# Kernel optimization log

Measured on AMD Instinct MI355X. Metric: run time of the kernel, lower is better.

The kernel has to match this reference:

```python
import jax, jax.numpy as jnp
import numpy as np

B, H, W = 64, 512, 512
T = 100           # num_thresholds
R = 8             # defect regions per image (max label id)
BLOCK = 128       # defect regions are 128x128 blocks on a 4x4 grid
SAT = 1.0         # saturation_threshold (relative)


def setup_inputs() -> dict:
    key = jax.random.key(0)
    k1, _ = jax.random.split(key)
    preds = jax.random.uniform(k1, (B, H, W), dtype=jnp.float32)
    thresholds = jnp.linspace(0.0, 1.0, T).astype(jnp.float32)
    # Build a labeled GT mask: R disjoint 128x128 block regions per image,
    # labels 1..R (0 = background). This plays the role of measure.label(target).
    rng = np.random.default_rng(0)
    labels = np.zeros((B, H, W), dtype=np.int32)
    gb = H // BLOCK           # 4 blocks per side -> 16 candidate blocks
    nblocks = gb * gb
    for b in range(B):
        chosen = rng.permutation(nblocks)[:R]
        for rid, blk in enumerate(chosen, start=1):
            r, c = divmod(int(blk), gb)
            labels[b, r * BLOCK:(r + 1) * BLOCK, c * BLOCK:(c + 1) * BLOCK] = rid
    return {"preds": preds, "thresholds": thresholds, "labels": jnp.asarray(labels)}


def reference(preds, thresholds, labels):
    # preds: (B,H,W) float32 in [0,1); thresholds: (T,) sorted; labels: (B,H,W) int32, 0=bg.
    Bn, Hn, Wn = preds.shape
    Tn = thresholds.shape[0]
    flat_s = preds.reshape(-1)
    flat_l = labels.reshape(-1)
    # bucket[p] = number of thresholds <= score[p]; pixel passes thr[t] iff bucket > t.
    bucket = jnp.searchsorted(thresholds, flat_s, side='right')  # int in [0, T]
    # ---- background FP / TN per threshold (exact counts via histogram) ----
    bg = (flat_l == 0).astype(jnp.int32)
    bg_hist = jax.ops.segment_sum(bg, bucket, num_segments=Tn + 1)  # (T+1,)
    bg_total = bg_hist.sum()
    fp = (bg_total - jnp.cumsum(bg_hist)[:Tn]).astype(jnp.float32)  # fp[t] = #bg with score>=thr[t]
    tn = bg_total.astype(jnp.float32) - fp
    # ---- per-region TP per threshold (segmented histogram) ----
    bidx = jnp.repeat(jnp.arange(Bn), Hn * Wn)
    seg = bidx * R + (flat_l - 1)              # region id in [0, B*R)
    comb = seg * (Tn + 1) + bucket
    NSEG = Bn * R * (Tn + 1)
    comb = jnp.where(flat_l > 0, comb, NSEG)   # dump bg pixels in overflow slot
    hist = jax.ops.segment_sum(jnp.ones_like(bucket, dtype=jnp.int32), comb,
                               num_segments=NSEG + 1)[:NSEG].reshape(Bn, R, Tn + 1)
    area = hist.sum(-1)                                       # (B,R) defect areas
    tp = (area[..., None] - jnp.cumsum(hist, -1)[..., :Tn]).astype(jnp.float32)  # (B,R,T)
    sat = jnp.maximum(area.astype(jnp.float32) * SAT, 1.0)    # relative saturation
    valid = (area > 0).astype(jnp.float32)                    # guard empty regions
    spro = jnp.minimum(tp / sat[..., None], 1.0) * valid[..., None]
    spro_sum = spro.sum((0, 1))                               # (T,)
    n_def = jnp.maximum(valid.sum(), 1.0)
    mean_spro = spro_sum / n_def
    # ---- AUC over FPR (max_fpr = 1.0) ----
    denom = fp + tn
    fpr = jnp.where(denom > 0, fp / jnp.maximum(denom, 1.0), 0.0)
    order = jnp.argsort(fpr)
    x = fpr[order]
    y = mean_spro[order]
    auc = jnp.sum((x[1:] - x[:-1]) * (y[1:] + y[:-1]) * 0.5)  # trapezoid rule
    return auc
```

## Files before the change

### kernel.cpp

```cpp
#include <hip/hip_runtime.h>

#define B_N 64
#define H_N 512
#define W_N 512
#define T_N 100
#define TB  101
#define R_N 8
#define NLAB 9
#define BLOCKS_PER_IMG 32
#define PIX_PER_IMG (H_N * W_N)
#define PIX_PER_BLOCK (PIX_PER_IMG / BLOCKS_PER_IMG)

__device__ __forceinline__ int bucket_of(float s) {
    const double C = 1.0 / 99.0;
    int k0 = (int)(s * 99.0f) + 1;
    float tlo = (float)((double)(k0 - 1) * C);
    float thi = (float)((double)k0 * C);
    return k0 - (s < tlo ? 1 : 0) + (s >= thi ? 1 : 0);
}

__global__ __launch_bounds__(256) void hist_kernel(
    const float* __restrict__ preds, const int* __restrict__ labels,
    int* __restrict__ region_hist,
    int* __restrict__ bg_hist)
{
    __shared__ int whist[4][NLAB * TB];

    const int tid  = threadIdx.x;
    const int wave = tid >> 6;

    for (int i = tid; i < 4 * NLAB * TB; i += 256) ((int*)whist)[i] = 0;
    __syncthreads();

    const int img   = blockIdx.x / BLOCKS_PER_IMG;
    const int chunk = blockIdx.x % BLOCKS_PER_IMG;
    const long base = (long)img * PIX_PER_IMG + (long)chunk * PIX_PER_BLOCK;
    const float4* p4 = (const float4*)(preds + base);
    const int4*   l4 = (const int4*)(labels + base);
    int* __restrict__ myh = whist[wave];

    const int iters = PIX_PER_BLOCK / (256 * 8);

    float4 pa = p4[tid], pb = p4[256 + tid];
    int4   la = l4[tid], lb = l4[256 + tid];
    for (int it = 0; it < iters; ++it) {
        float4 na, nb; int4 nla, nlb;
        if (it + 1 < iters) {
            int o = (it * 2 + 2) * 256 + tid;
            na  = p4[o]; nb  = p4[o + 256];
            nla = l4[o]; nlb = l4[o + 256];
        }
        float ps[8] = {pa.x, pa.y, pa.z, pa.w, pb.x, pb.y, pb.z, pb.w};
        int   ls[8] = {la.x, la.y, la.z, la.w, lb.x, lb.y, lb.z, lb.w};
#pragma unroll
        for (int j = 0; j < 8; ++j)
            atomicAdd(&myh[ls[j] * TB + bucket_of(ps[j])], 1);
        pa = na; pb = nb; la = nla; lb = nlb;
    }
    __syncthreads();

    for (int i = tid; i < NLAB * TB; i += 256) {
        int v = whist[0][i] + whist[1][i] + whist[2][i] + whist[3][i];
        if (v) {
            int lab = i / TB;
            int t   = i - lab * TB;
            if (lab == 0)
                atomicAdd(&bg_hist[img * TB + t], v);
            else
                atomicAdd(&region_hist[(img * R_N + (lab - 1)) * TB + t], v);
        }
    }
}

__global__ __launch_bounds__(256) void post_kernel(
    const int* __restrict__ region_hist,
    const int* __restrict__ bg_hist,
    float* __restrict__ spro_sum,
    int* __restrict__ n_def,
    int* __restrict__ done_ctr,
    float* __restrict__ out)
{
    __shared__ int   h_sh[R_N * TB];
    __shared__ float area_sh[R_N];
    __shared__ int   last_sh;
    const int img = blockIdx.x;
    const int tid = threadIdx.x;

    for (int i = tid; i < R_N * TB; i += 256)
        h_sh[i] = region_hist[img * (R_N * TB) + i];
    __syncthreads();

    if (tid < R_N) {
        int a = 0;
        for (int t = 0; t < TB; ++t) a += h_sh[tid * TB + t];
        area_sh[tid] = (float)a;
    }
    __syncthreads();

    if (tid < T_N) {
        float s = 0.0f;
#pragma unroll
        for (int r = 0; r < R_N; ++r) {
            int tp = 0;
            for (int k = tid + 1; k < TB; ++k) tp += h_sh[r * TB + k];
            float area  = area_sh[r];
            float sat   = fmaxf(area, 1.0f);
            float valid = (area > 0.0f) ? 1.0f : 0.0f;
            s += fminf((float)tp / sat, 1.0f) * valid;
        }
        atomicAdd(&spro_sum[tid], s);
    }
    if (tid == 0) {
        int v = 0;
        for (int r = 0; r < R_N; ++r) v += (area_sh[r] > 0.0f) ? 1 : 0;
        atomicAdd(n_def, v);
    }

    __syncthreads();
    if (tid == 0) {
        int prev = __hip_atomic_fetch_add(done_ctr, 1, __ATOMIC_ACQ_REL,
                                          __HIP_MEMORY_SCOPE_AGENT);
        last_sh = (prev == B_N - 1) ? 1 : 0;
    }
    __syncthreads();
    if (!last_sh) return;

    __shared__ int    stage[B_N * TB];
    __shared__ int    bgh[TB];
    __shared__ float  fpr_sh[T_N];
    __shared__ float  ms_sh[T_N];
    __shared__ int    order[T_N];
    __shared__ double contrib[T_N];

    for (int i = tid; i < B_N * TB; i += 256) stage[i] = bg_hist[i];
    __syncthreads();

    if (tid < TB) {
        int s = 0;
        for (int b = 0; b < B_N; ++b) s += stage[b * TB + tid];
        bgh[tid] = s;
    }
    __syncthreads();

    if (tid < T_N) {
        int fp_i = 0;
        for (int k = tid + 1; k < TB; ++k) fp_i += bgh[k];
        int tot = fp_i;
        for (int k = 0; k <= tid; ++k) tot += bgh[k];
        float bgt = (float)tot;
        float fp  = (float)fp_i;
        fpr_sh[tid] = (bgt > 0.0f) ? fp / fmaxf(bgt, 1.0f) : 0.0f;
        int   ndi = __hip_atomic_load(n_def, __ATOMIC_RELAXED, __HIP_MEMORY_SCOPE_AGENT);
        float ss  = __hip_atomic_load(&spro_sum[tid], __ATOMIC_RELAXED, __HIP_MEMORY_SCOPE_AGENT);
        float nd  = fmaxf((float)ndi, 1.0f);
        ms_sh[tid] = ss / nd;
    }
    __syncthreads();

    if (tid < T_N) {
        float v = fpr_sh[tid];
        int r = 0;
        for (int j = 0; j < T_N; ++j) {
            float u = fpr_sh[j];
            r += (u < v) | ((u == v) & (j < tid));
        }
        order[r] = tid;
    }
    __syncthreads();

    if (tid < T_N - 1) {
        int o0 = order[tid], o1 = order[tid + 1];
        double x0 = fpr_sh[o0], x1 = fpr_sh[o1];
        double y0 = ms_sh[o0],  y1 = ms_sh[o1];
        contrib[tid] = (x1 - x0) * (y0 + y1) * 0.5;
    } else if (tid < T_N) {
        contrib[tid] = 0.0;
    }
    __syncthreads();

    if (tid == 0) {
        double s = 0.0;
        for (int i = 0; i < T_N - 1; ++i) s += contrib[i];
        out[0] = (float)s;
    }
}

extern "C" void kernel_launch(void* const* d_in, const int* in_sizes, int n_in,
                              void* d_out, int out_size, void* d_ws, size_t ws_size,
                              hipStream_t stream) {
    const float* preds  = (const float*)d_in[0];
    const int*   labels = (const int*)d_in[2];
    float* out = (float*)d_out;

    int*   region_hist = (int*)d_ws;
    int*   bg_hist     = region_hist + B_N * R_N * TB;
    float* spro_sum    = (float*)(bg_hist + B_N * TB);
    int*   n_def       = (int*)(spro_sum + T_N);
    int*   done_ctr    = n_def + 1;

    size_t zbytes = sizeof(int) * (size_t)(B_N * R_N * TB + B_N * TB)
                  + sizeof(float) * T_N + 2 * sizeof(int);
    hipMemsetAsync(d_ws, 0, zbytes, stream);

    hist_kernel<<<B_N * BLOCKS_PER_IMG, 256, 0, stream>>>(preds, labels,
                                                          region_hist, bg_hist);
    post_kernel<<<B_N, 256, 0, stream>>>(region_hist, bg_hist, spro_sum,
                                         n_def, done_ctr, out);
}
```

Measured before the change: 168.1 us.

## Fuse histogram and post-processing into one cooperative kernel with grid syncs

Replaces the memset plus two kernel launches with a single cooperative kernel of 512 blocks. Each block zeroes part of the workspace, builds its shared-memory histogram, and the blocks then flush, reduce per image and compute the AUC between grid-wide syncs. This removes the launch and memset overhead and the last-block atomic counter. In exchange, each block now handles four times as many pixels, the software prefetch in the histogram loop is dropped, and three grid barriers are added. If the cooperative launch fails, a two-kernel path runs instead.

```diff
diff --git a/kernel.cpp b/kernel.cpp
--- a/kernel.cpp
+++ b/kernel.cpp
@@ -1,4 +1,7 @@
 #include <hip/hip_runtime.h>
+#include <hip/hip_cooperative_groups.h>
+
+namespace cg = cooperative_groups;
 
 #define B_N 64
 #define H_N 512
@@ -7,9 +10,15 @@
 #define TB  101
 #define R_N 8
 #define NLAB 9
-#define BLOCKS_PER_IMG 32
+#define NCOL (NLAB * TB)
 #define PIX_PER_IMG (H_N * W_N)
-#define PIX_PER_BLOCK (PIX_PER_IMG / BLOCKS_PER_IMG)
+
+#define CBLK_PER_IMG 8
+#define CGRID (B_N * CBLK_PER_IMG)
+#define CPIX (PIX_PER_IMG / CBLK_PER_IMG)
+#define FBLK_PER_IMG 32
+#define FGRID (B_N * FBLK_PER_IMG)
+#define FPIX (PIX_PER_IMG / FBLK_PER_IMG)
 
 __device__ __forceinline__ int bucket_of(float s) {
     const double C = 1.0 / 99.0;
@@ -19,144 +28,30 @@
     return k0 - (s < tlo ? 1 : 0) + (s >= thi ? 1 : 0);
 }
 
-__global__ __launch_bounds__(256) void hist_kernel(
-    const float* __restrict__ preds, const int* __restrict__ labels,
-    int* __restrict__ region_hist,
-    int* __restrict__ bg_hist)
-{
-    __shared__ int whist[4][NLAB * TB];
-
-    const int tid  = threadIdx.x;
-    const int wave = tid >> 6;
-
-    for (int i = tid; i < 4 * NLAB * TB; i += 256) ((int*)whist)[i] = 0;
-    __syncthreads();
-
-    const int img   = blockIdx.x / BLOCKS_PER_IMG;
-    const int chunk = blockIdx.x % BLOCKS_PER_IMG;
-    const long base = (long)img * PIX_PER_IMG + (long)chunk * PIX_PER_BLOCK;
+__device__ __forceinline__ void hist_phase(const float* __restrict__ preds,
+                                           const int* __restrict__ labels,
+                                           int* smem, int tid, int wave,
+                                           long base, int pix) {
     const float4* p4 = (const float4*)(preds + base);
     const int4*   l4 = (const int4*)(labels + base);
-    int* __restrict__ myh = whist[wave];
-
-    const int iters = PIX_PER_BLOCK / (256 * 8);
-
-    float4 pa = p4[tid], pb = p4[256 + tid];
-    int4   la = l4[tid], lb = l4[256 + tid];
+    int* myh = smem + wave * NCOL;
+    const int iters = pix / (256 * 8);
     for (int it = 0; it < iters; ++it) {
-        float4 na, nb; int4 nla, nlb;
-        if (it + 1 < iters) {
-            int o = (it * 2 + 2) * 256 + tid;
-            na  = p4[o]; nb  = p4[o + 256];
-            nla = l4[o]; nlb = l4[o + 256];
-        }
+        float4 pa = p4[(it * 2 + 0) * 256 + tid];
+        float4 pb = p4[(it * 2 + 1) * 256 + tid];
+        int4   la = l4[(it * 2 + 0) * 256 + tid];
+        int4   lb = l4[(it * 2 + 1) * 256 + tid];
         float ps[8] = {pa.x, pa.y, pa.z, pa.w, pb.x, pb.y, pb.z, pb.w};
         int   ls[8] = {la.x, la.y, la.z, la.w, lb.x, lb.y, lb.z, lb.w};
 #pragma unroll
         for (int j = 0; j < 8; ++j)
             atomicAdd(&myh[ls[j] * TB + bucket_of(ps[j])], 1);
-        pa = na; pb = nb; la = nla; lb = nlb;
-    }
-    __syncthreads();
-
-    for (int i = tid; i < NLAB * TB; i += 256) {
-        int v = whist[0][i] + whist[1][i] + whist[2][i] + whist[3][i];
-        if (v) {
-            int lab = i / TB;
-            int t   = i - lab * TB;
-            if (lab == 0)
-                atomicAdd(&bg_hist[img * TB + t], v);
-            else
-                atomicAdd(&region_hist[(img * R_N + (lab - 1)) * TB + t], v);
-        }
-    }
-}
-
-__global__ __launch_bounds__(256) void post_kernel(
-    const int* __restrict__ region_hist,
-    const int* __restrict__ bg_hist,
-    float* __restrict__ spro_sum,
-    int* __restrict__ n_def,
-    int* __restrict__ done_ctr,
-    float* __restrict__ out)
-{
-    __shared__ int   h_sh[R_N * TB];
-    __shared__ float area_sh[R_N];
-    __shared__ int   last_sh;
-    const int img = blockIdx.x;
-    const int tid = threadIdx.x;
-
-    for (int i = tid; i < R_N * TB; i += 256)
-        h_sh[i] = region_hist[img * (R_N * TB) + i];
-    __syncthreads();
-
-    if (tid < R_N) {
-        int a = 0;
-        for (int t = 0; t < TB; ++t) a += h_sh[tid * TB + t];
-        area_sh[tid] = (float)a;
-    }
-    __syncthreads();
-
-    if (tid < T_N) {
-        float s = 0.0f;
-#pragma unroll
-        for (int r = 0; r < R_N; ++r) {
-            int tp = 0;
-            for (int k = tid + 1; k < TB; ++k) tp += h_sh[r * TB + k];
-            float area  = area_sh[r];
-            float sat   = fmaxf(area, 1.0f);
-            float valid = (area > 0.0f) ? 1.0f : 0.0f;
-            s += fminf((float)tp / sat, 1.0f) * valid;
-        }
-        atomicAdd(&spro_sum[tid], s);
-    }
-    if (tid == 0) {
-        int v = 0;
-        for (int r = 0; r < R_N; ++r) v += (area_sh[r] > 0.0f) ? 1 : 0;
-        atomicAdd(n_def, v);
-    }
-
-    __syncthreads();
-    if (tid == 0) {
-        int prev = __hip_atomic_fetch_add(done_ctr, 1, __ATOMIC_ACQ_REL,
-                                          __HIP_MEMORY_SCOPE_AGENT);
-        last_sh = (prev == B_N - 1) ? 1 : 0;
-    }
-    __syncthreads();
-    if (!last_sh) return;
-
-    __shared__ int    stage[B_N * TB];
-    __shared__ int    bgh[TB];
-    __shared__ float  fpr_sh[T_N];
-    __shared__ float  ms_sh[T_N];
-    __shared__ int    order[T_N];
-    __shared__ double contrib[T_N];
-
-    for (int i = tid; i < B_N * TB; i += 256) stage[i] = bg_hist[i];
-    __syncthreads();
-
-    if (tid < TB) {
-        int s = 0;
-        for (int b = 0; b < B_N; ++b) s += stage[b * TB + tid];
-        bgh[tid] = s;
-    }
-    __syncthreads();
-
-    if (tid < T_N) {
-        int fp_i = 0;
-        for (int k = tid + 1; k < TB; ++k) fp_i += bgh[k];
-        int tot = fp_i;
-        for (int k = 0; k <= tid; ++k) tot += bgh[k];
-        float bgt = (float)tot;
-        float fp  = (float)fp_i;
-        fpr_sh[tid] = (bgt > 0.0f) ? fp / fmaxf(bgt, 1.0f) : 0.0f;
-        int   ndi = __hip_atomic_load(n_def, __ATOMIC_RELAXED, __HIP_MEMORY_SCOPE_AGENT);
-        float ss  = __hip_atomic_load(&spro_sum[tid], __ATOMIC_RELAXED, __HIP_MEMORY_SCOPE_AGENT);
-        float nd  = fmaxf((float)ndi, 1.0f);
-        ms_sh[tid] = ss / nd;
-    }
-    __syncthreads();
-
+    }
+}
+
+__device__ __forceinline__ void rank_sort_auc(int tid, const float* fpr_sh,
+                                              const float* ms_sh, int* order,
+                                              double* contrib, float* out) {
     if (tid < T_N) {
         float v = fpr_sh[tid];
         int r = 0;
@@ -167,7 +62,6 @@
         order[r] = tid;
     }
     __syncthreads();
-
     if (tid < T_N - 1) {
         int o0 = order[tid], o1 = order[tid + 1];
         double x0 = fpr_sh[o0], x1 = fpr_sh[o1];
@@ -177,12 +71,208 @@
         contrib[tid] = 0.0;
     }
     __syncthreads();
-
     if (tid == 0) {
         double s = 0.0;
         for (int i = 0; i < T_N - 1; ++i) s += contrib[i];
         out[0] = (float)s;
     }
+}
+
+__global__ __launch_bounds__(256) void fused_kernel(
+    const float* __restrict__ preds, const int* __restrict__ labels,
+    int*   __restrict__ rhist,
+    float* __restrict__ spro_part,
+    int*   __restrict__ validc,
+    float* __restrict__ out)
+{
+    cg::grid_group gg = cg::this_grid();
+    __shared__ __align__(16) int smem[4 * NCOL];
+
+    const int tid  = threadIdx.x;
+    const int bid  = blockIdx.x;
+    const int wave = tid >> 6;
+    const int gtid = bid * 256 + tid;
+
+    if (gtid < B_N * NCOL) rhist[gtid] = 0;
+
+    for (int i = tid; i < 4 * NCOL; i += 256) smem[i] = 0;
+    __syncthreads();
+
+    const int img   = bid / CBLK_PER_IMG;
+    const int chunk = bid % CBLK_PER_IMG;
+    hist_phase(preds, labels, smem, tid, wave,
+               (long)img * PIX_PER_IMG + (long)chunk * CPIX, CPIX);
+    __syncthreads();
+
+    gg.sync();
+
+    for (int i = tid; i < NCOL; i += 256) {
+        int v = smem[i] + smem[NCOL + i] + smem[2 * NCOL + i] + smem[3 * NCOL + i];
+        if (v) atomicAdd(&rhist[img * NCOL + i], v);
+    }
+
+    gg.sync();
+
+    if (bid < B_N) {
+        int*   h_sh    = smem;
+        float* area_sh = (float*)(smem + 912);
+        for (int i = tid; i < NCOL; i += 256) h_sh[i] = rhist[bid * NCOL + i];
+        __syncthreads();
+        if (tid < R_N) {
+            int a = 0;
+            for (int t = 0; t < TB; ++t) a += h_sh[(tid + 1) * TB + t];
+            area_sh[tid] = (float)a;
+        }
+        __syncthreads();
+        if (tid < T_N) {
+            float s = 0.0f;
+#pragma unroll
+            for (int r = 0; r < R_N; ++r) {
+                int tp = 0;
+                for (int k = tid + 1; k < TB; ++k) tp += h_sh[(r + 1) * TB + k];
+                float area  = area_sh[r];
+                float sat   = fmaxf(area, 1.0f);
+                float valid = (area > 0.0f) ? 1.0f : 0.0f;
+                s += fminf((float)tp / sat, 1.0f) * valid;
+            }
+            spro_part[bid * T_N + tid] = s;
+        }
+        if (tid == 0) {
+            int v = 0;
+            for (int r = 0; r < R_N; ++r) v += (area_sh[r] > 0.0f) ? 1 : 0;
+            validc[bid] = v;
+        }
+    }
+
+    gg.sync();
+
+    if (bid == 0) {
+        int*    bgh     = smem;
+        float*  ssum_sh = (float*)(smem + 104);
+        float*  fpr_sh  = (float*)(smem + 204);
+        float*  ms_sh   = (float*)(smem + 304);
+        int*    order   = smem + 404;
+        double* contrib = (double*)(smem + 504);
+        int*    ndef_sh = smem + 704;
+
+        if (tid < TB)  bgh[tid] = 0;
+        if (tid < T_N) ssum_sh[tid] = 0.0f;
+        if (tid == 0)  ndef_sh[0] = 0;
+        __syncthreads();
+
+        for (int i = tid; i < B_N * TB; i += 256) {
+            int b = i / TB, t = i - b * TB;
+            atomicAdd(&bgh[t], rhist[b * NCOL + t]);
+        }
+        for (int i = tid; i < B_N * T_N; i += 256)
+            atomicAdd(&ssum_sh[i % T_N], spro_part[i]);
+        if (tid < B_N) atomicAdd(ndef_sh, validc[tid]);
+        __syncthreads();
+
+        if (tid < T_N) {
+            int fp_i = 0;
+            for (int k = tid + 1; k < TB; ++k) fp_i += bgh[k];
+            int tot = fp_i;
+            for (int k = 0; k <= tid; ++k) tot += bgh[k];
+            float bgt = (float)tot;
+            fpr_sh[tid] = (bgt > 0.0f) ? (float)fp_i / fmaxf(bgt, 1.0f) : 0.0f;
+            float nd = fmaxf((float)ndef_sh[0], 1.0f);
+            ms_sh[tid] = ssum_sh[tid] / nd;
+        }
+        __syncthreads();
+
+        rank_sort_auc(tid, fpr_sh, ms_sh, order, contrib, out);
+    }
+}
+
+__global__ __launch_bounds__(256) void hist_kernel_fb(
+    const float* __restrict__ preds, const int* __restrict__ labels,
+    int* __restrict__ rhist)
+{
+    __shared__ __align__(16) int smem[4 * NCOL];
+    const int tid = threadIdx.x, wave = tid >> 6;
+    for (int i = tid; i < 4 * NCOL; i += 256) smem[i] = 0;
+    __syncthreads();
+    const int img   = blockIdx.x / FBLK_PER_IMG;
+    const int chunk = blockIdx.x % FBLK_PER_IMG;
+    hist_phase(preds, labels, smem, tid, wave,
+               (long)img * PIX_PER_IMG + (long)chunk * FPIX, FPIX);
+    __syncthreads();
+    for (int i = tid; i < NCOL; i += 256) {
+        int v = smem[i] + smem[NCOL + i] + smem[2 * NCOL + i] + smem[3 * NCOL + i];
+        if (v) atomicAdd(&rhist[img * NCOL + i], v);
+    }
+}
+
+__global__ __launch_bounds__(256) void post_kernel_fb(
+    const int* __restrict__ rhist, float* __restrict__ spro_sum,
+    int* __restrict__ n_def, int* __restrict__ done_ctr,
+    float* __restrict__ out)
+{
+    __shared__ int   h_sh[NCOL];
+    __shared__ float area_sh[R_N];
+    __shared__ int   last_sh;
+    const int img = blockIdx.x, tid = threadIdx.x;
+
+    for (int i = tid; i < NCOL; i += 256) h_sh[i] = rhist[img * NCOL + i];
+    __syncthreads();
+    if (tid < R_N) {
+        int a = 0;
+        for (int t = 0; t < TB; ++t) a += h_sh[(tid + 1) * TB + t];
+        area_sh[tid] = (float)a;
+    }
+    __syncthreads();
+    if (tid < T_N) {
+        float s = 0.0f;
+#pragma unroll
+        for (int r = 0; r < R_N; ++r) {
+            int tp = 0;
+            for (int k = tid + 1; k < TB; ++k) tp += h_sh[(r + 1) * TB + k];
+            float area  = area_sh[r];
+            float sat   = fmaxf(area, 1.0f);
+            float valid = (area > 0.0f) ? 1.0f : 0.0f;
+            s += fminf((float)tp / sat, 1.0f) * valid;
+        }
+        atomicAdd(&spro_sum[tid], s);
+    }
+    if (tid == 0) {
+        int v = 0;
+        for (int r = 0; r < R_N; ++r) v += (area_sh[r] > 0.0f) ? 1 : 0;
+        atomicAdd(n_def, v);
+    }
+    __syncthreads();
+    if (tid == 0) {
+        int prev = __hip_atomic_fetch_add(done_ctr, 1, __ATOMIC_ACQ_REL,
+                                          __HIP_MEMORY_SCOPE_AGENT);
+        last_sh = (prev == B_N - 1) ? 1 : 0;
+    }
+    __syncthreads();
+    if (!last_sh) return;
+
+    __shared__ int    bgh[TB];
+    __shared__ float  fpr_sh[T_N], ms_sh[T_N];
+    __shared__ int    order[T_N];
+    __shared__ double contrib[T_N];
+    if (tid < TB) bgh[tid] = 0;
+    __syncthreads();
+    for (int i = tid; i < B_N * TB; i += 256) {
+        int b = i / TB, t = i - b * TB;
+        atomicAdd(&bgh[t], rhist[b * NCOL + t]);
+    }
+    __syncthreads();
+    if (tid < T_N) {
+        int fp_i = 0;
+        for (int k = tid + 1; k < TB; ++k) fp_i += bgh[k];
+        int tot = fp_i;
+        for (int k = 0; k <= tid; ++k) tot += bgh[k];
+        float bgt = (float)tot;
+        fpr_sh[tid] = (bgt > 0.0f) ? (float)fp_i / fmaxf(bgt, 1.0f) : 0.0f;
+        int   ndi = __hip_atomic_load(n_def, __ATOMIC_RELAXED, __HIP_MEMORY_SCOPE_AGENT);
+        float ss  = __hip_atomic_load(&spro_sum[tid], __ATOMIC_RELAXED, __HIP_MEMORY_SCOPE_AGENT);
+        ms_sh[tid] = ss / fmaxf((float)ndi, 1.0f);
+    }
+    __syncthreads();
+    rank_sort_auc(tid, fpr_sh, ms_sh, order, contrib, out);
 }
 
 extern "C" void kernel_launch(void* const* d_in, const int* in_sizes, int n_in,
@@ -192,18 +282,24 @@
     const int*   labels = (const int*)d_in[2];
     float* out = (float*)d_out;
 
-    int*   region_hist = (int*)d_ws;
-    int*   bg_hist     = region_hist + B_N * R_N * TB;
-    float* spro_sum    = (float*)(bg_hist + B_N * TB);
-    int*   n_def       = (int*)(spro_sum + T_N);
-    int*   done_ctr    = n_def + 1;
-
-    size_t zbytes = sizeof(int) * (size_t)(B_N * R_N * TB + B_N * TB)
-                  + sizeof(float) * T_N + 2 * sizeof(int);
-    hipMemsetAsync(d_ws, 0, zbytes, stream);
-
-    hist_kernel<<<B_N * BLOCKS_PER_IMG, 256, 0, stream>>>(preds, labels,
-                                                          region_hist, bg_hist);
-    post_kernel<<<B_N, 256, 0, stream>>>(region_hist, bg_hist, spro_sum,
-                                         n_def, done_ctr, out);
-}
+    int*   rhist     = (int*)d_ws;
+    float* spro_sum  = (float*)(rhist + B_N * NCOL);
+    int*   n_def     = (int*)(spro_sum + T_N);
+    int*   done_ctr  = n_def + 1;
+    float* spro_part = (float*)(done_ctr + 1);
+    int*   validc    = (int*)(spro_part + B_N * T_N);
+
+    void* args[] = { (void*)&preds, (void*)&labels, (void*)&rhist,
+                     (void*)&spro_part, (void*)&validc, (void*)&out };
+    hipError_t e = hipLaunchCooperativeKernel((const void*)fused_kernel,
+                                              dim3(CGRID), dim3(256), args, 0, stream);
+    if (e != hipSuccess) {
+        (void)hipGetLastError();
+        size_t zbytes = sizeof(int) * (size_t)(B_N * NCOL) + sizeof(float) * T_N
+                      + 2 * sizeof(int);
+        hipMemsetAsync(d_ws, 0, zbytes, stream);
+        hist_kernel_fb<<<FGRID, 256, 0, stream>>>(preds, labels, rhist);
+        post_kernel_fb<<<B_N, 256, 0, stream>>>(rhist, spro_sum, n_def,
+                                                done_ctr, out);
+    }
+}
```

Result: slower. 339.8 us (+102.1%).
